# Kernel tuning notes

Measured on AMD Instinct MI355X. Metric: run time of the kernel, lower is better.

## Reference

```python
import jax, jax.numpy as jnp
import numpy as np

# Hierarchy from the source module: super-class -> list of fine sub-classes
HIERARCHY_MAP = {0: [0, 1], 1: [2, 3, 4, 5, 6, 7, 8], 2: [9, 10, 11, 12, 13], 3: [14, 15]}
NUM_CLASSES = 16
N = 2_097_152  # batch size; logits are 128 MB fp32
EPS = 1e-8


def setup_inputs() -> dict:
    key = jax.random.key(0)
    k1, k2, k3 = jax.random.split(key, 3)
    logits = jax.random.normal(k1, (N, NUM_CLASSES), dtype=jnp.float32)
    # targets in [0, 4): valid both as fine-class indices and super-class indices
    remapped_targets = jax.random.randint(k2, (N,), 0, 4, dtype=jnp.int32)
    is_fine = jax.random.randint(k3, (N,), 0, 2, dtype=jnp.int32)  # 1 -> 'fine', 0 -> 'coarse'
    # Membership matrix M[s, c] = 1 if fine class c belongs to super class s
    mask = np.zeros((len(HIERARCHY_MAP), NUM_CLASSES), dtype=np.float32)
    for s, subs in HIERARCHY_MAP.items():
        mask[s, subs] = 1.0
    return {
        "logits": logits,
        "remapped_targets": remapped_targets,
        "is_fine": is_fine,
        "super_mask": jnp.asarray(mask),
    }


def reference(logits, remapped_targets, is_fine, super_mask):
    # log-softmax over classes, numerically stable, computed once
    log_probs = jax.nn.log_softmax(logits, axis=1)  # [N, C]
    # fine branch: -log p[target]
    fine_nll = -jnp.take_along_axis(log_probs, remapped_targets[:, None], axis=1)[:, 0]  # [N]
    # coarse branch: -log(sum_{c in subclasses(target)} p[c] + eps)
    mask_rows = super_mask[remapped_targets]  # [N, C] gather of membership rows
    coarse_nll = -jnp.log(jnp.sum(jnp.exp(log_probs) * mask_rows, axis=1) + EPS)  # [N]
    per_sample = jnp.where(is_fine == 1, fine_nll, coarse_nll)
    return jnp.mean(per_sample)
```

## Files before the change

kernel.cpp:

```cpp
#include <hip/hip_runtime.h>
#include <hip/hip_bf16.h>


#define ROWS_PER_ITER 64
#define ITERS 8
#define ROWS_PER_BLOCK (ROWS_PER_ITER * ITERS)

__global__ __launch_bounds__(256) void hce_main(
    const float* __restrict__ logits,
    const int* __restrict__ targets,
    const int* __restrict__ is_fine,
    const float* __restrict__ super_mask,
    double* __restrict__ acc,
    int N)
{
    const int t = threadIdx.x;
    const int sub = t & 3;
    const int rbase = blockIdx.x * ROWS_PER_BLOCK + (t >> 2);

    const float4* __restrict__ lg4 = (const float4*)logits;
    const float4* __restrict__ mk4 = (const float4*)super_mask;

    float local = 0.0f;

    #pragma unroll
    for (int i = 0; i < ITERS; ++i) {
        const int row = rbase + i * ROWS_PER_ITER;
        if (row < N) {
            float4 v = lg4[row * 4 + sub];

            float m = fmaxf(fmaxf(v.x, v.y), fmaxf(v.z, v.w));
            m = fmaxf(m, __shfl_xor(m, 1));
            m = fmaxf(m, __shfl_xor(m, 2));

            float e0 = __expf(v.x - m);
            float e1 = __expf(v.y - m);
            float e2 = __expf(v.z - m);
            float e3 = __expf(v.w - m);

            float s = e0 + e1 + e2 + e3;
            s += __shfl_xor(s, 1);
            s += __shfl_xor(s, 2);

            const int tgt = targets[row];
            const int fin = is_fine[row];

            float4 mk = mk4[tgt * 4 + sub];
            float ms = mk.x * e0 + mk.y * e1 + mk.z * e2 + mk.w * e3;
            ms += __shfl_xor(ms, 1);
            ms += __shfl_xor(ms, 2);

            float comp = (tgt & 1) ? ((tgt & 2) ? v.w : v.y)
                                   : ((tgt & 2) ? v.z : v.x);
            float lt = ((tgt >> 2) == sub) ? comp : 0.0f;
            lt += __shfl_xor(lt, 1);
            lt += __shfl_xor(lt, 2);

            float logS = __logf(s);
            float fine_nll   = m + logS - lt;
            float coarse_nll = -__logf(ms / s + 1e-8f);

            float per = (fin == 1) ? fine_nll : coarse_nll;
            if (sub == 0) local += per;
        }
    }

    #pragma unroll
    for (int off = 1; off < 64; off <<= 1)
        local += __shfl_xor(local, off);

    __shared__ float wsum[4];
    const int wave = t >> 6;
    if ((t & 63) == 0) wsum[wave] = local;
    __syncthreads();
    if (t == 0) {
        float blockSum = wsum[0] + wsum[1] + wsum[2] + wsum[3];
        atomicAdd(acc, (double)blockSum);
    }
}

__global__ void hce_finalize(const double* __restrict__ acc,
                             float* __restrict__ out, int N)
{
    out[0] = (float)(acc[0] / (double)N);
}

extern "C" void kernel_launch(void* const* d_in, const int* in_sizes, int n_in,
                              void* d_out, int out_size, void* d_ws, size_t ws_size,
                              hipStream_t stream)
{
    const float* logits     = (const float*)d_in[0];
    const int*   targets    = (const int*)d_in[1];
    const int*   is_fine    = (const int*)d_in[2];
    const float* super_mask = (const float*)d_in[3];
    float*       out        = (float*)d_out;
    double*      acc        = (double*)d_ws;

    const int N = in_sizes[1];

    hipMemsetAsync(acc, 0, sizeof(double), stream);

    const int blocks = (N + ROWS_PER_BLOCK - 1) / ROWS_PER_BLOCK;
    hce_main<<<blocks, 256, 0, stream>>>(logits, targets, is_fine, super_mask, acc, N);
    hce_finalize<<<1, 1, 0, stream>>>(acc, out, N);
}
```

Measured before the change: 230.9 us.

## Assign one full row per thread instead of four threads per row

```diff
diff --git a/kernel.cpp b/kernel.cpp
--- a/kernel.cpp
+++ b/kernel.cpp
@@ -2,11 +2,11 @@
 #include <hip/hip_bf16.h>
 
 
-#define ROWS_PER_ITER 64
-#define ITERS 8
-#define ROWS_PER_BLOCK (ROWS_PER_ITER * ITERS)
+#define TPB 256
+#define RPT 8
+#define ROWS_PER_BLOCK (TPB * RPT)
 
-__global__ __launch_bounds__(256) void hce_main(
+__global__ __launch_bounds__(TPB) void hce_main(
     const float* __restrict__ logits,
     const int* __restrict__ targets,
     const int* __restrict__ is_fine,
@@ -15,8 +15,7 @@
     int N)
 {
     const int t = threadIdx.x;
-    const int sub = t & 3;
-    const int rbase = blockIdx.x * ROWS_PER_BLOCK + (t >> 2);
+    const int base = blockIdx.x * ROWS_PER_BLOCK + t;
 
     const float4* __restrict__ lg4 = (const float4*)logits;
     const float4* __restrict__ mk4 = (const float4*)super_mask;
@@ -24,44 +23,54 @@
     float local = 0.0f;
 
     #pragma unroll
-    for (int i = 0; i < ITERS; ++i) {
-        const int row = rbase + i * ROWS_PER_ITER;
+    for (int k = 0; k < RPT; ++k) {
+        const int row = base + k * TPB;
         if (row < N) {
-            float4 v = lg4[row * 4 + sub];
+            float4 a = lg4[row * 4 + 0];
+            float4 b = lg4[row * 4 + 1];
+            float4 c = lg4[row * 4 + 2];
+            float4 d = lg4[row * 4 + 3];
 
-            float m = fmaxf(fmaxf(v.x, v.y), fmaxf(v.z, v.w));
-            m = fmaxf(m, __shfl_xor(m, 1));
-            m = fmaxf(m, __shfl_xor(m, 2));
+            float m = fmaxf(fmaxf(fmaxf(a.x, a.y), fmaxf(a.z, a.w)),
+                     fmaxf(fmaxf(fmaxf(b.x, b.y), fmaxf(b.z, b.w)),
+                     fmaxf(fmaxf(fmaxf(c.x, c.y), fmaxf(c.z, c.w)),
+                           fmaxf(fmaxf(d.x, d.y), fmaxf(d.z, d.w)))));
 
-            float e0 = __expf(v.x - m);
-            float e1 = __expf(v.y - m);
-            float e2 = __expf(v.z - m);
-            float e3 = __expf(v.w - m);
+            float ea0 = __expf(a.x - m), ea1 = __expf(a.y - m);
+            float ea2 = __expf(a.z - m), ea3 = __expf(a.w - m);
+            float eb0 = __expf(b.x - m), eb1 = __expf(b.y - m);
+            float eb2 = __expf(b.z - m), eb3 = __expf(b.w - m);
+            float ec0 = __expf(c.x - m), ec1 = __expf(c.y - m);
+            float ec2 = __expf(c.z - m), ec3 = __expf(c.w - m);
+            float ed0 = __expf(d.x - m), ed1 = __expf(d.y - m);
+            float ed2 = __expf(d.z - m), ed3 = __expf(d.w - m);
 
-            float s = e0 + e1 + e2 + e3;
-            s += __shfl_xor(s, 1);
-            s += __shfl_xor(s, 2);
+            float s = (ea0 + ea1 + ea2 + ea3) + (eb0 + eb1 + eb2 + eb3)
+                    + (ec0 + ec1 + ec2 + ec3) + (ed0 + ed1 + ed2 + ed3);
 
             const int tgt = targets[row];
             const int fin = is_fine[row];
 
-            float4 mk = mk4[tgt * 4 + sub];
-            float ms = mk.x * e0 + mk.y * e1 + mk.z * e2 + mk.w * e3;
-            ms += __shfl_xor(ms, 1);
-            ms += __shfl_xor(ms, 2);
+            float4 m0 = mk4[tgt * 4 + 0];
+            float4 m1 = mk4[tgt * 4 + 1];
+            float4 m2 = mk4[tgt * 4 + 2];
+            float4 m3 = mk4[tgt * 4 + 3];
+            float ms = m0.x*ea0 + m0.y*ea1 + m0.z*ea2 + m0.w*ea3
+                     + m1.x*eb0 + m1.y*eb1 + m1.z*eb2 + m1.w*eb3
+                     + m2.x*ec0 + m2.y*ec1 + m2.z*ec2 + m2.w*ec3
+                     + m3.x*ed0 + m3.y*ed1 + m3.z*ed2 + m3.w*ed3;
 
-            float comp = (tgt & 1) ? ((tgt & 2) ? v.w : v.y)
-                                   : ((tgt & 2) ? v.z : v.x);
-            float lt = ((tgt >> 2) == sub) ? comp : 0.0f;
-            lt += __shfl_xor(lt, 1);
-            lt += __shfl_xor(lt, 2);
+            const int q = tgt >> 2, r = tgt & 3;
+            float4 vq;
+            vq = (q & 2) ? ((q & 1) ? d : c) : ((q & 1) ? b : a);
+            float lt = (r & 2) ? ((r & 1) ? vq.w : vq.z)
+                               : ((r & 1) ? vq.y : vq.x);
 
             float logS = __logf(s);
             float fine_nll   = m + logS - lt;
             float coarse_nll = -__logf(ms / s + 1e-8f);
 
-            float per = (fin == 1) ? fine_nll : coarse_nll;
-            if (sub == 0) local += per;
+            local += (fin == 1) ? fine_nll : coarse_nll;
         }
     }
 
@@ -69,12 +78,14 @@
     for (int off = 1; off < 64; off <<= 1)
         local += __shfl_xor(local, off);
 
-    __shared__ float wsum[4];
+    __shared__ float wsum[TPB / 64];
     const int wave = t >> 6;
     if ((t & 63) == 0) wsum[wave] = local;
     __syncthreads();
     if (t == 0) {
-        float blockSum = wsum[0] + wsum[1] + wsum[2] + wsum[3];
+        float blockSum = 0.0f;
+        #pragma unroll
+        for (int w = 0; w < TPB / 64; ++w) blockSum += wsum[w];
         atomicAdd(acc, (double)blockSum);
     }
 }
@@ -101,6 +112,6 @@
     hipMemsetAsync(acc, 0, sizeof(double), stream);
 
     const int blocks = (N + ROWS_PER_BLOCK - 1) / ROWS_PER_BLOCK;
-    hce_main<<<blocks, 256, 0, stream>>>(logits, targets, is_fine, super_mask, acc, N);
+    hce_main<<<blocks, TPB, 0, stream>>>(logits, targets, is_fine, super_mask, acc, N);
     hce_finalize<<<1, 1, 0, stream>>>(acc, out, N);
 }
```

Result: faster. 214.1 us (-7.3%).
